# Performance work log

Hardware: AMD Instinct MI355X
Metric: run time of the kernel (lower is better)

The kernel has to match this reference:

```python
import jax, jax.numpy as jnp
import numpy as np

B, P, HID = 2, 4096, 1152
N_HEADS, HEAD_DIM = 16, 72
EPS = 1e-6


def _rms_norm(x, w=None):
    # x fp32; normalize over last dim
    ms = jnp.mean(x * x, axis=-1, keepdims=True) + EPS
    y = x * jax.lax.rsqrt(ms)
    if w is not None:
        y = y * w
    return y


def _rotate_half(x):
    d = x.shape[-1] // 2
    return jnp.concatenate([-x[..., d:], x[..., :d]], axis=-1)


def _apply_rotary(x, c, s):
    # x: [B,P,N,d], c/s: [B,P,d] -> broadcast over heads
    c = c[:, :, None, :]
    s = s[:, :, None, :]
    return x * c + _rotate_half(x) * s


def _multidim_rope(x, cos, sin, ndim=2):
    per = x.shape[-1] // ndim
    parts = []
    for k in range(ndim):
        sl = slice(k * per, (k + 1) * per)
        parts.append(_apply_rotary(x[..., sl], cos[..., sl], sin[..., sl]))
    return jnp.concatenate(parts, axis=-1)


def setup_inputs() -> dict:
    key = jax.random.key(0)
    ks = jax.random.split(key, 8)
    return {
        "hidden_states": jax.random.normal(ks[0], (B, P, HID), jnp.float32),
        "cos": jax.random.normal(ks[1], (B, P, HEAD_DIM), jnp.float32),
        "sin": jax.random.normal(ks[2], (B, P, HEAD_DIM), jnp.float32),
        "Wq": jax.random.normal(ks[3], (HID, N_HEADS * HEAD_DIM), jnp.float32) * 0.02,
        "Wk": jax.random.normal(ks[4], (HID, N_HEADS * HEAD_DIM), jnp.float32) * 0.02,
        "Wv": jax.random.normal(ks[5], (HID, N_HEADS * HEAD_DIM), jnp.float32) * 0.02,
        "Wo": jax.random.normal(ks[6], (N_HEADS * HEAD_DIM, HID), jnp.float32) * 0.02,
        "q_norm_w": jnp.ones((HEAD_DIM,), jnp.float32),
        "k_norm_w": jnp.ones((HEAD_DIM,), jnp.float32),
    }


def reference(hidden_states, cos, sin, Wq, Wk, Wv, Wo, q_norm_w, k_norm_w):
    b, p, _ = hidden_states.shape
    q = (hidden_states @ Wq).reshape(b, p, N_HEADS, HEAD_DIM)
    k = (hidden_states @ Wk).reshape(b, p, N_HEADS, HEAD_DIM)
    v = (hidden_states @ Wv).reshape(b, p, N_HEADS, HEAD_DIM)
    # per-head RMSNorm (q/k with learned scale, v without)
    q = _rms_norm(q, q_norm_w)
    k = _rms_norm(k, k_norm_w)
    v = _rms_norm(v)
    # multi-dim RoPE (ndim=2)
    q = _multidim_rope(q, cos, sin)
    k = _multidim_rope(k, cos, sin)
    # attention, scaling = 1.0, no mask (non-causal vision)
    scores = jnp.einsum('bqnd,bknd->bnqk', q, k)  # [B,N,P,P]
    attn = jax.nn.softmax(scores.astype(jnp.float32), axis=-1).astype(q.dtype)
    out = jnp.einsum('bnqk,bknd->bqnd', attn, v).reshape(b, p, N_HEADS * HEAD_DIM)
    return out @ Wo
```

## Files before the change

kernel.cpp:

```cpp
#include <hip/hip_runtime.h>
#include <stdint.h>

typedef __attribute__((ext_vector_type(8))) _Float16 half8;
typedef __attribute__((ext_vector_type(4))) _Float16 half4;
typedef __attribute__((ext_vector_type(4))) float floatx4;

#define NHEADS 16
#define HDIM   72
#define DPAD   80
#define DPADV  80
#define HID    1152
#define NQKV   3456
#define PP     4096
#define MR     8192
#define LOG2E  1.44269504f

__device__ __forceinline__ float bf2f(unsigned short u) {
  union { unsigned int i; float f; } c; c.i = ((unsigned int)u) << 16; return c.f;
}
__device__ __forceinline__ unsigned short f2bf(float f) {
  union { float f; unsigned int i; } c; c.f = f;
  unsigned int x = c.i;
  x += ((x >> 16) & 1u) + 0x7fffu;
  return (unsigned short)(x >> 16);
}
__device__ __forceinline__ float load_in(const void* p, long long i, int bf) {
  return bf ? bf2f(((const unsigned short*)p)[i]) : ((const float*)p)[i];
}

__global__ __launch_bounds__(64) void k_detect(const void* hs, int* flag) {
  int lane = threadIdx.x;
  const unsigned short* u = (const unsigned short*)hs;
  int wild = 0;
  for (int t = 0; t < 8; ++t) {
    unsigned short v = u[lane * 8 + t];
    int e = (v >> 7) & 0xFF;
    if (e >= 134) wild++;
  }
  for (int off = 1; off < 64; off <<= 1) wild += __shfl_xor(wild, off);
  if (lane == 0) flag[0] = (wild > 32) ? 0 : 1;
}

__global__ __launch_bounds__(256) void k_prep(
    const void* hs, const void* cosp, const void* sinp,
    const void* wq, const void* wk, const void* wv, const void* wo,
    const void* qnw, const void* knw, const int* flag,
    _Float16* Xh, _Float16* Wqkv, _Float16* Wot,
    float* cosf, float* sinf, float* qw, float* kw) {
  int bf = flag[0];
  long long i = (long long)blockIdx.x * blockDim.x + threadIdx.x;
  const long long n0 = (long long)MR * HID;
  const long long n1 = (long long)NQKV * HID;
  const long long n2 = (long long)HID * HID;
  const long long n3 = (long long)2 * PP * HDIM;
  if (i < n0) { Xh[i] = (_Float16)load_in(hs, i, bf); return; }
  i -= n0;
  if (i < n1) {
    long long n = i / HID, kk = i - n * HID;
    int sel = (int)(n / HID);
    long long nl = n - (long long)sel * HID;
    const void* W = (sel == 0) ? wq : ((sel == 1) ? wk : wv);
    Wqkv[i] = (_Float16)load_in(W, kk * HID + nl, bf);
    return;
  }
  i -= n1;
  if (i < n2) {
    long long n = i / HID, kk = i - n * HID;
    Wot[i] = (_Float16)load_in(wo, kk * HID + n, bf);
    return;
  }
  i -= n2;
  if (i < n3) { cosf[i] = load_in(cosp, i, bf); return; }
  i -= n3;
  if (i < n3) { sinf[i] = load_in(sinp, i, bf); return; }
  i -= n3;
  if (i < HDIM) { qw[i] = load_in(qnw, i, bf); return; }
  i -= HDIM;
  if (i < HDIM) { kw[i] = load_in(knw, i, bf); return; }
}

#define LDA 40
__global__ __launch_bounds__(256) void k_gemm(
    const _Float16* __restrict__ A, const _Float16* __restrict__ Bt,
    int N, int K, int mode, const int* __restrict__ flag,
    void* __restrict__ outp) {
  __shared__ _Float16 As[128 * LDA];
  __shared__ _Float16 Bs[128 * LDA];
  int tid = threadIdx.x;
  int wave = tid >> 6, lane = tid & 63;
  int quad = lane >> 4, l16 = lane & 15;

  int lin = blockIdx.y * gridDim.x + blockIdx.x;
  int xcd = lin & 7;
  int j = lin >> 3;
  int nbx = gridDim.x;
  int rows_per = gridDim.y >> 3;
  int by = xcd * rows_per + j / nbx;
  int bx = j - (j / nbx) * nbx;
  int bM = by * 128, bN = bx * 128;

  int wm = (wave & 1) * 64, wn = (wave >> 1) * 64;
  int qk = quad * 8;
  int sr = tid >> 1, sc = (tid & 1) * 16;

  floatx4 acc[4][4];
  floatx4 z4 = {0.f, 0.f, 0.f, 0.f};
#pragma unroll
  for (int i = 0; i < 4; ++i)
#pragma unroll
    for (int jj = 0; jj < 4; ++jj) acc[i][jj] = z4;

  const _Float16* gA = A + (size_t)(bM + sr) * K + sc;
  const _Float16* gB = Bt + (size_t)(bN + sr) * K + sc;

  half8 a0 = *(const half8*)(gA);
  half8 a1 = *(const half8*)(gA + 8);
  half8 b0 = *(const half8*)(gB);
  half8 b1 = *(const half8*)(gB + 8);
  gA += 32; gB += 32;

  for (int k0 = 0; k0 < K; k0 += 32) {
    __syncthreads();
    *(half8*)(As + sr * LDA + sc)     = a0;
    *(half8*)(As + sr * LDA + sc + 8) = a1;
    *(half8*)(Bs + sr * LDA + sc)     = b0;
    *(half8*)(Bs + sr * LDA + sc + 8) = b1;
    __syncthreads();
    if (k0 + 32 < K) {
      a0 = *(const half8*)(gA);
      a1 = *(const half8*)(gA + 8);
      b0 = *(const half8*)(gB);
      b1 = *(const half8*)(gB + 8);
      gA += 32; gB += 32;
    }
    half8 af[4], bfv[4];
#pragma unroll
    for (int i = 0; i < 4; ++i)
      af[i] = *(const half8*)(As + (wm + i * 16 + l16) * LDA + qk);
#pragma unroll
    for (int jj = 0; jj < 4; ++jj)
      bfv[jj] = *(const half8*)(Bs + (wn + jj * 16 + l16) * LDA + qk);
#pragma unroll
    for (int i = 0; i < 4; ++i)
#pragma unroll
      for (int jj = 0; jj < 4; ++jj)
        acc[i][jj] = __builtin_amdgcn_mfma_f32_16x16x32_f16(af[i], bfv[jj], acc[i][jj], 0, 0, 0);
  }

  if (mode == 0) {
#pragma unroll
    for (int i = 0; i < 4; ++i)
#pragma unroll
      for (int jj = 0; jj < 4; ++jj)
#pragma unroll
        for (int r = 0; r < 4; ++r) {
          size_t row = (size_t)(bM + wm + i * 16 + quad * 4 + r);
          size_t col = (size_t)(bN + wn + jj * 16 + l16);
          ((_Float16*)outp)[row * N + col] = (_Float16)acc[i][jj][r];
        }
  } else {
    int obf = flag[0];
#pragma unroll
    for (int i = 0; i < 4; ++i)
#pragma unroll
      for (int jj = 0; jj < 4; ++jj)
#pragma unroll
        for (int r = 0; r < 4; ++r) {
          size_t row = (size_t)(bM + wm + i * 16 + quad * 4 + r);
          size_t col = (size_t)(bN + wn + jj * 16 + l16);
          float v = acc[i][jj][r];
          if (obf) ((unsigned short*)outp)[row * N + col] = f2bf(v);
          else     ((float*)outp)[row * N + col] = v;
        }
  }
}

__global__ __launch_bounds__(256) void k_norm_rope(
    const _Float16* __restrict__ QKV, const float* __restrict__ cosf,
    const float* __restrict__ sinf, const float* __restrict__ qw,
    const float* __restrict__ kw,
    _Float16* __restrict__ Qp, _Float16* __restrict__ Kp,
    _Float16* __restrict__ Vp) {
  int wave = threadIdx.x >> 6, lane = threadIdx.x & 63;
  int bid = blockIdx.x * 4 + wave;
  int m = bid >> 4, h = bid & 15;
  int b = m >> 12, p = m & 4095;
  __shared__ float sq[4][HDIM], sk[4][HDIM];

  const _Float16* rowp = QKV + (long long)m * NQKV + h * HDIM;
  int i0 = lane, i1 = lane + 64;
  bool has1 = (i1 < HDIM);
  float q0 = (float)rowp[i0];
  float k0 = (float)rowp[1152 + i0];
  float v0 = (float)rowp[2304 + i0];
  float q1 = 0.f, k1 = 0.f, v1 = 0.f;
  if (has1) { q1 = (float)rowp[i1]; k1 = (float)rowp[1152 + i1]; v1 = (float)rowp[2304 + i1]; }

  float sq_s = q0 * q0 + q1 * q1;
  float sk_s = k0 * k0 + k1 * k1;
  float sv_s = v0 * v0 + v1 * v1;
  for (int off = 1; off < 64; off <<= 1) {
    sq_s += __shfl_xor(sq_s, off);
    sk_s += __shfl_xor(sk_s, off);
    sv_s += __shfl_xor(sv_s, off);
  }
  float rq = rsqrtf(sq_s / 72.f + 1e-6f);
  float rk = rsqrtf(sk_s / 72.f + 1e-6f);
  float rv = rsqrtf(sv_s / 72.f + 1e-6f);

  sq[wave][i0] = q0 * rq * qw[i0];
  sk[wave][i0] = k0 * rk * kw[i0];
  if (has1) { sq[wave][i1] = q1 * rq * qw[i1]; sk[wave][i1] = k1 * rk * kw[i1]; }
  __syncthreads();

  const float* crow = cosf + (long long)m * HDIM;
  const float* srow = sinf + (long long)m * HDIM;
  long long obase = ((long long)(b * NHEADS + h) * PP + p) * DPAD;
  long long obV   = ((long long)(b * NHEADS + h) * PP + p) * DPADV;
#pragma unroll
  for (int t = 0; t < 2; ++t) {
    int i = lane + t * 64;
    if (i < DPAD) {
      _Float16 qv = (_Float16)0.f, kv = (_Float16)0.f;
      if (i < HDIM) {
        int j = (i >= 36) ? (i - 36) : i;
        float c = crow[i], s = srow[i];
        float qo, ko;
        if (j < 18) { qo = sq[wave][i] * c - sq[wave][i + 18] * s; ko = sk[wave][i] * c - sk[wave][i + 18] * s; }
        else        { qo = sq[wave][i] * c + sq[wave][i - 18] * s; ko = sk[wave][i] * c + sk[wave][i - 18] * s; }
        qv = (_Float16)(qo * LOG2E); kv = (_Float16)ko;
      }
      Qp[obase + i] = qv; Kp[obase + i] = kv;
    }
    if (i < DPADV) {
      _Float16 vv = (_Float16)0.f;
      if (i < HDIM) vv = (_Float16)(((t == 0) ? v0 : v1) * rv);
      Vp[obV + i] = vv;
    }
  }
}

__global__ __launch_bounds__(256) void k_vtrans(
    const _Float16* __restrict__ Vp, _Float16* __restrict__ VtG) {
  __shared__ _Float16 T[DPADV * 72];
  int tid = threadIdx.x;
  int pt = blockIdx.x, bh = blockIdx.y;
  long long src = (long long)bh * PP * DPADV + (long long)pt * 64 * DPADV;
#pragma unroll
  for (int pp = 0; pp < 3; ++pp) {
    int c = tid + pp * 256;
    if (c < 640) {
      int r = c / 10, ds = c % 10;
      half8 v = *(const half8*)(Vp + src + r * DPADV + ds * 8);
#pragma unroll
      for (int j = 0; j < 8; ++j) T[(ds * 8 + j) * 72 + r] = v[j];
    }
  }
  __syncthreads();
  long long dst = (long long)bh * DPADV * PP + (long long)pt * 64;
#pragma unroll
  for (int pp = 0; pp < 3; ++pp) {
    int c = tid + pp * 256;
    if (c < 640) {
      int d = c >> 3, ps = (c & 7) * 8;
      half8 v = *(const half8*)(T + d * 72 + ps);
      if (d == 72) {
#pragma unroll
        for (int j = 0; j < 8; ++j) v[j] = (_Float16)1.f;
      }
      *(half8*)(VtG + dst + (long long)d * PP + ps) = v;
    }
  }
}

#define TK 64
#define NT (PP / TK)
#define LDK 80
#define LDV 72
__global__ __launch_bounds__(256) void k_flash(
    const _Float16* __restrict__ Qp, const _Float16* __restrict__ Kp,
    const _Float16* __restrict__ VtG, _Float16* __restrict__ Oat) {
  __shared__ _Float16 Kl[TK * LDK];
  __shared__ _Float16 Vt[DPADV * LDV];
  __shared__ _Float16 Pl[128 * LDV];
  int tid = threadIdx.x, wave = tid >> 6, lane = tid & 63;
  int quad = lane >> 4, l16 = lane & 15;
  int bh = blockIdx.x, qt = blockIdx.y;
  const long long headoff = (long long)bh * PP * DPAD;
  const long long vhead   = (long long)bh * DPADV * PP;

  half8 zh8;
#pragma unroll
  for (int j = 0; j < 8; ++j) zh8[j] = (_Float16)0.f;

  half8 qf[2][3];
#pragma unroll
  for (int mb = 0; mb < 2; ++mb) {
    int qrow = qt * 128 + wave * 32 + mb * 16 + l16;
    const _Float16* qp = Qp + headoff + (long long)qrow * DPAD;
#pragma unroll
    for (int ck = 0; ck < 2; ++ck)
      qf[mb][ck] = *(const half8*)(qp + ck * 32 + quad * 8);
    qf[mb][2] = zh8;
    if (quad < 2) qf[mb][2] = *(const half8*)(qp + 64 + quad * 8);
  }

  floatx4 O[2][5];
  floatx4 z4 = {0.f, 0.f, 0.f, 0.f};
#pragma unroll
  for (int mb = 0; mb < 2; ++mb)
#pragma unroll
    for (int d = 0; d < 5; ++d) O[mb][d] = z4;
  float m_i[2];
  m_i[0] = -1e30f; m_i[1] = -1e30f;
  _Float16* Pw = Pl + wave * 32 * LDV;

  half8 kreg[3], vreg[3];
  {
    const _Float16* Ksrc = Kp + headoff;
    const _Float16* Vsrc = VtG + vhead;
#pragma unroll
    for (int pp = 0; pp < 3; ++pp) {
      int c = tid + pp * 256;
      if (c < 640)
        kreg[pp] = *(const half8*)(Ksrc + c * 8);
    }
#pragma unroll
    for (int pp = 0; pp < 3; ++pp) {
      int c = tid + pp * 256;
      if (c < 640)
        vreg[pp] = *(const half8*)(Vsrc + (long long)(c >> 3) * PP + (c & 7) * 8);
    }
  }

  for (int kt = 0; kt < NT; ++kt) {
    __syncthreads();
#pragma unroll
    for (int pp = 0; pp < 3; ++pp) {
      int c = tid + pp * 256;
      if (c < 640)
        *(half8*)(Kl + (c / 10) * LDK + (c % 10) * 8) = kreg[pp];
    }
#pragma unroll
    for (int pp = 0; pp < 3; ++pp) {
      int c = tid + pp * 256;
      if (c < 640)
        *(half8*)(Vt + (c >> 3) * LDV + (c & 7) * 8) = vreg[pp];
    }
    __syncthreads();

    {
      int ktn = (kt + 1 < NT) ? kt + 1 : kt;
      const _Float16* Ksrc = Kp + headoff + (long long)ktn * TK * DPAD;
      const _Float16* Vsrc = VtG + vhead + ktn * TK;
#pragma unroll
      for (int pp = 0; pp < 3; ++pp) {
        int c = tid + pp * 256;
        if (c < 640)
          kreg[pp] = *(const half8*)(Ksrc + c * 8);
      }
#pragma unroll
      for (int pp = 0; pp < 3; ++pp) {
        int c = tid + pp * 256;
        if (c < 640)
          vreg[pp] = *(const half8*)(Vsrc + (long long)(c >> 3) * PP + (c & 7) * 8);
      }
    }

    floatx4 sb[2][4];
    __builtin_amdgcn_s_setprio(1);
#pragma unroll
    for (int nb = 0; nb < 4; ++nb) {
      const _Float16* kp = Kl + (nb * 16 + l16) * LDK;
      half8 kf0 = *(const half8*)(kp + quad * 8);
      half8 kf1 = *(const half8*)(kp + 32 + quad * 8);
      half8 kf2 = zh8;
      if (quad < 2) kf2 = *(const half8*)(kp + 64 + quad * 8);
#pragma unroll
      for (int mb = 0; mb < 2; ++mb) {
        floatx4 a = __builtin_amdgcn_mfma_f32_16x16x32_f16(kf0, qf[mb][0], z4, 0, 0, 0);
        a = __builtin_amdgcn_mfma_f32_16x16x32_f16(kf1, qf[mb][1], a, 0, 0, 0);
        a = __builtin_amdgcn_mfma_f32_16x16x32_f16(kf2, qf[mb][2], a, 0, 0, 0);
        sb[mb][nb] = a;
      }
    }
    __builtin_amdgcn_s_setprio(0);

#pragma unroll
    for (int mb = 0; mb < 2; ++mb) {
      float t = fmaxf(fmaxf(sb[mb][0][0], sb[mb][0][1]),
                      fmaxf(sb[mb][0][2], sb[mb][0][3]));
#pragma unroll
      for (int nb = 1; nb < 4; ++nb)
        t = fmaxf(t, fmaxf(fmaxf(sb[mb][nb][0], sb[mb][nb][1]),
                           fmaxf(sb[mb][nb][2], sb[mb][nb][3])));
      t = fmaxf(t, __shfl_xor(t, 16));
      t = fmaxf(t, __shfl_xor(t, 32));
      if (!__all(t <= m_i[mb] + 11.5f)) {
        float mnew = fmaxf(m_i[mb], t);
        float al = __builtin_amdgcn_exp2f(m_i[mb] - mnew);
        m_i[mb] = mnew;
        float alT[4];
#pragma unroll
        for (int r = 0; r < 4; ++r)
          alT[r] = __shfl(al, (lane & 48) + quad * 4 + r);
#pragma unroll
        for (int d = 0; d < 5; ++d)
#pragma unroll
          for (int r = 0; r < 4; ++r) O[mb][d][r] *= alT[r];
      }
      float mi = m_i[mb];
#pragma unroll
      for (int nb = 0; nb < 4; ++nb) {
        half4 w;
#pragma unroll
        for (int r = 0; r < 4; ++r)
          w[r] = (_Float16)__builtin_amdgcn_exp2f(sb[mb][nb][r] - mi);
        *(half4*)(Pw + (mb * 16 + l16) * LDV + nb * 16 + quad * 4) = w;
      }
    }

    __builtin_amdgcn_s_setprio(1);
#pragma unroll
    for (int ck2 = 0; ck2 < 2; ++ck2) {
      half8 pf0 = *(const half8*)(Pw + l16 * LDV + ck2 * 32 + quad * 8);
      half8 pf1 = *(const half8*)(Pw + (16 + l16) * LDV + ck2 * 32 + quad * 8);
#pragma unroll
      for (int d = 0; d < 5; ++d) {
        half8 vf = *(const half8*)(Vt + (d * 16 + l16) * LDV + ck2 * 32 + quad * 8);
        O[0][d] = __builtin_amdgcn_mfma_f32_16x16x32_f16(pf0, vf, O[0][d], 0, 0, 0);
        O[1][d] = __builtin_amdgcn_mfma_f32_16x16x32_f16(pf1, vf, O[1][d], 0, 0, 0);
      }
    }
    __builtin_amdgcn_s_setprio(0);
  }

  int b = bh >> 4, h = bh & 15;
  int src = (lane & 48) + 8;
#pragma unroll
  for (int mb = 0; mb < 2; ++mb) {
    float linv[4];
#pragma unroll
    for (int r = 0; r < 4; ++r)
      linv[r] = 1.f / __shfl(O[mb][4][r], src);
    long long orow = (long long)b * PP + qt * 128 + wave * 32 + mb * 16 + quad * 4;
#pragma unroll
    for (int d = 0; d < 5; ++d) {
      int dd = d * 16 + l16;
      if (dd < HDIM) {
#pragma unroll
        for (int r = 0; r < 4; ++r)
          Oat[(orow + r) * HID + h * HDIM + dd] = (_Float16)(O[mb][d][r] * linv[r]);
      }
    }
  }
}

extern "C" void kernel_launch(void* const* d_in, const int* in_sizes, int n_in,
                              void* d_out, int out_size, void* d_ws, size_t ws_size,
                              hipStream_t stream) {
  (void)in_sizes; (void)n_in; (void)out_size; (void)ws_size;
  const void* hs   = d_in[0];
  const void* cosp = d_in[1];
  const void* sinp = d_in[2];
  const void* wq   = d_in[3];
  const void* wk   = d_in[4];
  const void* wv   = d_in[5];
  const void* wo   = d_in[6];
  const void* qnw  = d_in[7];
  const void* knw  = d_in[8];

  char* ws = (char*)d_ws;
  size_t off = 0;
  auto take = [&](size_t bytes) -> char* {
    off = (off + 255) & ~(size_t)255;
    char* p = ws + off; off += bytes; return p;
  };
  int* flag        = (int*)take(4);
  _Float16* Xh     = (_Float16*)take((size_t)MR * HID * 2);
  _Float16* Wqkvh  = (_Float16*)take((size_t)NQKV * HID * 2);
  _Float16* Woth   = (_Float16*)take((size_t)HID * HID * 2);
  float* cosf_     = (float*)take((size_t)2 * PP * HDIM * 4);
  float* sinf_     = (float*)take((size_t)2 * PP * HDIM * 4);
  float* qwf       = (float*)take(HDIM * 4);
  float* kwf       = (float*)take(HDIM * 4);
  _Float16* QKVh   = (_Float16*)take((size_t)MR * NQKV * 2);
  _Float16* Kp     = (_Float16*)take((size_t)2 * NHEADS * PP * DPAD * 2);
  _Float16* Vp     = (_Float16*)take((size_t)2 * NHEADS * PP * DPADV * 2);
  _Float16* Qp  = Xh;
  _Float16* Oat = QKVh;
  _Float16* VtG = (_Float16*)((char*)QKVh + (size_t)20 * 1024 * 1024);

  k_detect<<<dim3(1), dim3(64), 0, stream>>>(hs, flag);

  long long totalPrep = (long long)MR * HID + (long long)NQKV * HID +
                        (long long)HID * HID + 2LL * 2 * PP * HDIM + 2 * HDIM;
  int prepBlocks = (int)((totalPrep + 255) / 256);
  k_prep<<<dim3(prepBlocks), dim3(256), 0, stream>>>(
      hs, cosp, sinp, wq, wk, wv, wo, qnw, knw, flag,
      Xh, Wqkvh, Woth, cosf_, sinf_, qwf, kwf);

  k_gemm<<<dim3(NQKV / 128, MR / 128), dim3(256), 0, stream>>>(
      Xh, Wqkvh, NQKV, HID, 0, flag, QKVh);

  k_norm_rope<<<dim3(MR * NHEADS / 4), dim3(256), 0, stream>>>(
      QKVh, cosf_, sinf_, qwf, kwf, Qp, Kp, Vp);

  k_vtrans<<<dim3(PP / 64, 2 * NHEADS), dim3(256), 0, stream>>>(Vp, VtG);

  k_flash<<<dim3(2 * NHEADS, PP / 128), dim3(256), 0, stream>>>(Qp, Kp, VtG, Oat);

  k_gemm<<<dim3(HID / 128, MR / 128), dim3(256), 0, stream>>>(
      Oat, Woth, HID, HID, 1, flag, d_out);
}
```

Measured before the change: 612.8 us.

## Load GEMM tiles directly into LDS and restructure attention row-max reduction

The GEMM kernel now fills its shared-memory tiles with global_load_lds direct-to-LDS transfers instead of staging them through registers. This drops the register prefetch double-buffering and the padded LDS stride (40 becomes 32). The aim is to cut VGPR pressure and the separate LDS store instructions, at the cost of losing the overlap from prefetching the next tile and of possible LDS bank conflicts with the unpadded layout. The attention kernel's row-max is also regrouped into three-operand fmax chains so it can map to max3 instructions.

New measurement: 631.9 us. 3.1% more time.

```diff
diff --git a/kernel.cpp b/kernel.cpp
--- a/kernel.cpp
+++ b/kernel.cpp
@@ -26,6 +26,12 @@
 }
 __device__ __forceinline__ float load_in(const void* p, long long i, int bf) {
   return bf ? bf2f(((const unsigned short*)p)[i]) : ((const float*)p)[i];
+}
+
+typedef const __attribute__((address_space(1))) void* gas_ptr;
+typedef __attribute__((address_space(3))) void* las_ptr;
+__device__ __forceinline__ void gload16(const _Float16* g, _Float16* l) {
+  __builtin_amdgcn_global_load_lds((gas_ptr)g, (las_ptr)l, 16, 0, 0);
 }
 
 __global__ __launch_bounds__(64) void k_detect(const void* hs, int* flag) {
@@ -79,13 +85,13 @@
   if (i < HDIM) { kw[i] = load_in(knw, i, bf); return; }
 }
 
-#define LDA 40
+#define BK 32
 __global__ __launch_bounds__(256) void k_gemm(
     const _Float16* __restrict__ A, const _Float16* __restrict__ Bt,
     int N, int K, int mode, const int* __restrict__ flag,
     void* __restrict__ outp) {
-  __shared__ _Float16 As[128 * LDA];
-  __shared__ _Float16 Bs[128 * LDA];
+  __shared__ _Float16 As[128 * BK];
+  __shared__ _Float16 Bs[128 * BK];
   int tid = threadIdx.x;
   int wave = tid >> 6, lane = tid & 63;
   int quad = lane >> 4, l16 = lane & 15;
@@ -101,7 +107,6 @@
 
   int wm = (wave & 1) * 64, wn = (wave >> 1) * 64;
   int qk = quad * 8;
-  int sr = tid >> 1, sc = (tid & 1) * 16;
 
   floatx4 acc[4][4];
   floatx4 z4 = {0.f, 0.f, 0.f, 0.f};
@@ -110,36 +115,29 @@
 #pragma unroll
     for (int jj = 0; jj < 4; ++jj) acc[i][jj] = z4;
 
-  const _Float16* gA = A + (size_t)(bM + sr) * K + sc;
-  const _Float16* gB = Bt + (size_t)(bN + sr) * K + sc;
-
-  half8 a0 = *(const half8*)(gA);
-  half8 a1 = *(const half8*)(gA + 8);
-  half8 b0 = *(const half8*)(gB);
-  half8 b1 = *(const half8*)(gB + 8);
-  gA += 32; gB += 32;
-
-  for (int k0 = 0; k0 < K; k0 += 32) {
+  const _Float16* gA0 = A  + (size_t)(bM + (tid >> 2)) * K + (tid & 3) * 8;
+  const _Float16* gB0 = Bt + (size_t)(bN + (tid >> 2)) * K + (tid & 3) * 8;
+  const _Float16* gA1 = gA0 + (size_t)64 * K;
+  const _Float16* gB1 = gB0 + (size_t)64 * K;
+  _Float16* lA = As + wave * 512;
+  _Float16* lB = Bs + wave * 512;
+
+  for (int k0 = 0; k0 < K; k0 += BK) {
     __syncthreads();
-    *(half8*)(As + sr * LDA + sc)     = a0;
-    *(half8*)(As + sr * LDA + sc + 8) = a1;
-    *(half8*)(Bs + sr * LDA + sc)     = b0;
-    *(half8*)(Bs + sr * LDA + sc + 8) = b1;
+    gload16(gA0, lA);
+    gload16(gA1, lA + 2048);
+    gload16(gB0, lB);
+    gload16(gB1, lB + 2048);
+    gA0 += BK; gA1 += BK; gB0 += BK; gB1 += BK;
     __syncthreads();
-    if (k0 + 32 < K) {
-      a0 = *(const half8*)(gA);
-      a1 = *(const half8*)(gA + 8);
-      b0 = *(const half8*)(gB);
-      b1 = *(const half8*)(gB + 8);
-      gA += 32; gB += 32;
-    }
+
     half8 af[4], bfv[4];
 #pragma unroll
     for (int i = 0; i < 4; ++i)
-      af[i] = *(const half8*)(As + (wm + i * 16 + l16) * LDA + qk);
+      af[i] = *(const half8*)(As + (wm + i * 16 + l16) * BK + qk);
 #pragma unroll
     for (int jj = 0; jj < 4; ++jj)
-      bfv[jj] = *(const half8*)(Bs + (wn + jj * 16 + l16) * LDA + qk);
+      bfv[jj] = *(const half8*)(Bs + (wn + jj * 16 + l16) * BK + qk);
 #pragma unroll
     for (int i = 0; i < 4; ++i)
 #pragma unroll
@@ -388,12 +386,14 @@
 
 #pragma unroll
     for (int mb = 0; mb < 2; ++mb) {
-      float t = fmaxf(fmaxf(sb[mb][0][0], sb[mb][0][1]),
-                      fmaxf(sb[mb][0][2], sb[mb][0][3]));
-#pragma unroll
-      for (int nb = 1; nb < 4; ++nb)
-        t = fmaxf(t, fmaxf(fmaxf(sb[mb][nb][0], sb[mb][nb][1]),
-                           fmaxf(sb[mb][nb][2], sb[mb][nb][3])));
+      float t1 = fmaxf(fmaxf(sb[mb][0][0], sb[mb][0][1]), sb[mb][0][2]);
+      float t2 = fmaxf(fmaxf(sb[mb][0][3], sb[mb][1][0]), sb[mb][1][1]);
+      float t3 = fmaxf(fmaxf(sb[mb][1][2], sb[mb][1][3]), sb[mb][2][0]);
+      float t4 = fmaxf(fmaxf(sb[mb][2][1], sb[mb][2][2]), sb[mb][2][3]);
+      float t5 = fmaxf(fmaxf(sb[mb][3][0], sb[mb][3][1]), sb[mb][3][2]);
+      float t = fmaxf(fmaxf(t1, t2), t3);
+      t = fmaxf(fmaxf(t, t4), t5);
+      t = fmaxf(t, sb[mb][3][3]);
       t = fmaxf(t, __shfl_xor(t, 16));
       t = fmaxf(t, __shfl_xor(t, 32));
       if (!__all(t <= m_i[mb] + 11.5f)) {
```
